# Kernel optimization log

Hardware: AMD Instinct MI355X
Metric: run time of the kernel (lower is better)

The kernel has to match this reference:

```python
import jax, jax.numpy as jnp
import numpy as np

DIM = 256
NUM_HEADS = 8
HEAD_DIM = DIM // NUM_HEADS          # 32
KEY_DIM = int(HEAD_DIM * 0.5)        # 16
SCALE = KEY_DIM ** (-0.5)
QKV_OUT = DIM + 2 * KEY_DIM * NUM_HEADS  # 512
BN_EPS = 1e-3


def _bn(x, gamma, beta, mean, var):
    # inference-mode BatchNorm2d over channel axis 1 of NCHW
    inv = gamma / jnp.sqrt(var + BN_EPS)
    return x * inv[None, :, None, None] + (beta - mean * inv)[None, :, None, None]


def _conv1x1(x, w):
    # w: (O, C, 1, 1)
    return jnp.einsum('bchw,oc->bohw', x, w[:, :, 0, 0])


def _dwconv3x3(x, w):
    # depthwise 3x3, SAME padding; w: (C, 1, 3, 3)
    return jax.lax.conv_general_dilated(
        x, w, window_strides=(1, 1), padding='SAME',
        feature_group_count=x.shape[1],
        dimension_numbers=('NCHW', 'OIHW', 'NCHW'))


def setup_inputs() -> dict:
    key = jax.random.key(0)
    ks = jax.random.split(key, 16)
    B, C, H, W = 16, DIM, 32, 32
    inp = {
        'x': jax.random.normal(ks[0], (B, C, H, W), jnp.float32),
        'qkv_w': jax.random.normal(ks[1], (QKV_OUT, DIM, 1, 1), jnp.float32) * (1.0 / np.sqrt(DIM)),
        'qkv_gamma': jnp.ones((QKV_OUT,), jnp.float32),
        'qkv_beta': jnp.zeros((QKV_OUT,), jnp.float32),
        'qkv_mean': jax.random.normal(ks[2], (QKV_OUT,), jnp.float32) * 0.1,
        'qkv_var': jax.random.uniform(ks[3], (QKV_OUT,), jnp.float32, 0.5, 1.5),
        'pe_w': jax.random.normal(ks[4], (DIM, 1, 3, 3), jnp.float32) * (1.0 / 3.0),
        'pe_gamma': jnp.ones((DIM,), jnp.float32),
        'pe_beta': jnp.zeros((DIM,), jnp.float32),
        'pe_mean': jax.random.normal(ks[5], (DIM,), jnp.float32) * 0.1,
        'pe_var': jax.random.uniform(ks[6], (DIM,), jnp.float32, 0.5, 1.5),
        'proj_w': jax.random.normal(ks[7], (DIM, DIM, 1, 1), jnp.float32) * (1.0 / np.sqrt(DIM)),
        'proj_gamma': jnp.ones((DIM,), jnp.float32),
        'proj_beta': jnp.zeros((DIM,), jnp.float32),
        'proj_mean': jax.random.normal(ks[8], (DIM,), jnp.float32) * 0.1,
        'proj_var': jax.random.uniform(ks[9], (DIM,), jnp.float32, 0.5, 1.5),
    }
    return inp


def reference(x, qkv_w, qkv_gamma, qkv_beta, qkv_mean, qkv_var,
              pe_w, pe_gamma, pe_beta, pe_mean, pe_var,
              proj_w, proj_gamma, proj_beta, proj_mean, proj_var):
    B, C, H, W = x.shape
    N = H * W
    # qkv: 1x1 conv + BN (act=False)
    qkv = _bn(_conv1x1(x, qkv_w), qkv_gamma, qkv_beta, qkv_mean, qkv_var)
    qkv = qkv.reshape(B, NUM_HEADS, 2 * KEY_DIM + HEAD_DIM, N)
    q = qkv[:, :, :KEY_DIM]                          # (B, h, kd, N)
    k = qkv[:, :, KEY_DIM:2 * KEY_DIM]               # (B, h, kd, N)
    v = qkv[:, :, 2 * KEY_DIM:]                      # (B, h, hd, N)
    # attn = (q^T @ k) * scale, softmax over last dim
    attn = jnp.einsum('bhdn,bhdm->bhnm', q, k) * SCALE   # (B, h, N, N)
    attn = jax.nn.softmax(attn, axis=-1)
    # v @ attn^T
    v_attn = jnp.einsum('bhdn,bhmn->bhdm', v, attn)      # (B, h, hd, N)
    v_attn = v_attn.reshape(B, C, H, W)
    v_reshaped = v.reshape(B, C, H, W)
    pos_enc = _bn(_dwconv3x3(v_reshaped, pe_w), pe_gamma, pe_beta, pe_mean, pe_var)
    out = v_attn + pos_enc
    out = _bn(_conv1x1(out, proj_w), proj_gamma, proj_beta, proj_mean, proj_var)
    return out
```

## Files before the change

kernel.cpp:

```cpp
#include <hip/hip_runtime.h>

#define B_ 16
#define C_ 256
#define N_ 1024
#define NH 8
#define HD 32
#define KD 16
#define QKV_OUT_ 512
#define BN_EPS 1e-3f
#define SCALE2_ (0.25f * 1.44269504088896f)

typedef __attribute__((ext_vector_type(8))) short short8;
typedef __attribute__((ext_vector_type(16))) float float16;

__device__ inline unsigned short f2bf(float f) {
  unsigned int u = __float_as_uint(f);
  return (unsigned short)((u + 0x7FFF + ((u >> 16) & 1)) >> 16);
}
__device__ inline float bf2f(unsigned short s) {
  return __uint_as_float(((unsigned int)s) << 16);
}
__device__ inline float16 zero16() {
  float16 z;
  #pragma unroll
  for (int i = 0; i < 16; ++i) z[i] = 0.f;
  return z;
}
__device__ inline unsigned int pack_bf16_trunc(float a, float b) {
  return __builtin_amdgcn_perm(__float_as_uint(b), __float_as_uint(a), 0x07060302u);
}
__device__ inline unsigned int pack_bf16_rne(float a, float b) {
  return (unsigned int)f2bf(a) | ((unsigned int)f2bf(b) << 16);
}
__device__ inline float fast_exp2(float x) {
#if __has_builtin(__builtin_amdgcn_exp2f)
  return __builtin_amdgcn_exp2f(x);
#else
  return exp2f(x);
#endif
}
__device__ inline void pl32(unsigned int& a, unsigned int& b) {
#if __has_builtin(__builtin_amdgcn_permlane32_swap)
  typedef __attribute__((ext_vector_type(2))) int int2v;
  int2v r = __builtin_amdgcn_permlane32_swap((int)a, (int)b, false, false);
  a = (unsigned int)r[0];
  b = (unsigned int)r[1];
#else
  unsigned int ea = (unsigned int)__shfl_xor((int)a, 32, 64);
  unsigned int eb = (unsigned int)__shfl_xor((int)b, 32, 64);
  bool hi = (threadIdx.x & 32) != 0;
  unsigned int an = hi ? eb : a;
  unsigned int bn = hi ? b : ea;
  a = an; b = bn;
#endif
}
__device__ inline short8 lds_frag(const unsigned short* p) {
  union { uint2 u[2]; short8 s; } r;
  r.u[0] = *(const uint2*)p;
  r.u[1] = *(const uint2*)(p + 4);
  return r.s;
}
__device__ inline void lds_store16(unsigned short* p, uint4 v) {
  *(uint2*)p = make_uint2(v.x, v.y);
  *(uint2*)(p + 4) = make_uint2(v.z, v.w);
}
__device__ inline void gl2lds16(const unsigned short* g, unsigned short* l) {
#if __has_builtin(__builtin_amdgcn_global_load_lds)
  __builtin_amdgcn_global_load_lds(
      (const __attribute__((address_space(1))) unsigned int*)g,
      (__attribute__((address_space(3))) unsigned int*)l, 16, 0, 0);
#else
  const int lane = threadIdx.x & 63;
  *(uint4*)((char*)l + lane * 16) = *(const uint4*)g;
#endif
}

__global__ __launch_bounds__(256) void fold_weights(
    const float* __restrict__ qkv_w, const float* __restrict__ qg,
    const float* __restrict__ qb, const float* __restrict__ qm,
    const float* __restrict__ qv,
    const float* __restrict__ proj_w, const float* __restrict__ pg,
    const float* __restrict__ pb, const float* __restrict__ pm,
    const float* __restrict__ pv,
    unsigned short* __restrict__ wq, float* __restrict__ biasq,
    unsigned short* __restrict__ wp, float* __restrict__ biasp)
{
  const int o = blockIdx.x, c = threadIdx.x;
  if (o < QKV_OUT_) {
    float s = ((o & 63) < 16) ? SCALE2_ : 1.f;
    float inv = qg[o] * rsqrtf(qv[o] + BN_EPS) * s;
    wq[o * C_ + c] = f2bf(qkv_w[o * C_ + c] * inv);
    if (c == 0) biasq[o] = qb[o] * s - qm[o] * inv;
  } else {
    int oo = o - QKV_OUT_;
    float inv = pg[oo] * rsqrtf(pv[oo] + BN_EPS);
    wp[oo * C_ + c] = f2bf(proj_w[oo * C_ + c] * inv);
    if (c == 0) biasp[oo] = pb[oo] - pm[oo] * inv;
  }
}

__global__ __launch_bounds__(256) void transpose_x(
    const float* __restrict__ x, unsigned short* __restrict__ xT)
{
  __shared__ float t[64][69];
  const int tid = threadIdx.x;
  const int nt = blockIdx.x, ct = blockIdx.y, b = blockIdx.z;
  const int n0 = nt * 64, c0 = ct * 64;

  #pragma unroll
  for (int it = 0; it < 4; ++it) {
    int cl = it * 16 + (tid >> 4);
    int nl = (tid & 15) * 4;
    float4 v = *(const float4*)(x + ((size_t)b * C_ + c0 + cl) * N_ + n0 + nl);
    t[cl][nl + 0] = v.x; t[cl][nl + 1] = v.y;
    t[cl][nl + 2] = v.z; t[cl][nl + 3] = v.w;
  }
  __syncthreads();

  const int nr = tid >> 2, cseg = (tid & 3) * 16;
  unsigned int pk[8];
  #pragma unroll
  for (int q = 0; q < 8; ++q)
    pk[q] = pack_bf16_rne(t[cseg + 2 * q][nr], t[cseg + 2 * q + 1][nr]);
  unsigned short* row = xT + ((size_t)b * N_ + n0 + nr) * C_ + c0 + cseg;
  *(uint4*)(row)     = make_uint4(pk[0], pk[1], pk[2], pk[3]);
  *(uint4*)(row + 8) = make_uint4(pk[4], pk[5], pk[6], pk[7]);
}

template <int MODE>
__global__ __launch_bounds__(256) void gemm_gl(
    const unsigned short* __restrict__ inT, const unsigned short* __restrict__ wfold,
    const float* __restrict__ bias,
    unsigned short* __restrict__ qkT, unsigned short* __restrict__ vbuf,
    float* __restrict__ outf)
{
  __shared__ __align__(16) unsigned short wa[128 * 64];
  __shared__ __align__(16) unsigned short xb[128 * 64];
  const int tid = threadIdx.x;
  const int wave = tid >> 6, lane = tid & 63, l31 = lane & 31, lh = lane >> 5;
  const int wm = wave & 1, wn = wave >> 1;
  const int n0g = blockIdx.x * 128;
  const int o0 = blockIdx.y * 128;
  const int b = n0g >> 10, nloc = n0g & 1023;

  const int crow = lane >> 3;
  const int cseg = (lane & 7) * 8;

  float16 acc[2][2];
  #pragma unroll
  for (int i = 0; i < 2; ++i)
    #pragma unroll
    for (int j = 0; j < 2; ++j) acc[i][j] = zero16();

  for (int kc = 0; kc < 4; ++kc) {
    __syncthreads();
    #pragma unroll
    for (int j = 0; j < 4; ++j) {
      const int rbase = wave * 32 + j * 8;
      const int row = rbase + crow;
      gl2lds16(wfold + (size_t)(o0 + row) * C_ + kc * 64 + cseg, &wa[rbase * 64]);
      gl2lds16(inT + (size_t)(n0g + row) * C_ + kc * 64 + cseg, &xb[rbase * 64]);
    }
    __syncthreads();

    #pragma unroll
    for (int ks = 0; ks < 4; ++ks) {
      const int ko = ks * 16 + lh * 8;
      short8 a0 = *(const short8*)&wa[(wm * 64 + l31) * 64 + ko];
      short8 a1 = *(const short8*)&wa[(wm * 64 + 32 + l31) * 64 + ko];
      short8 b0 = *(const short8*)&xb[(wn * 64 + l31) * 64 + ko];
      short8 b1 = *(const short8*)&xb[(wn * 64 + 32 + l31) * 64 + ko];
      acc[0][0] = __builtin_amdgcn_mfma_f32_32x32x16_bf16(a0, b0, acc[0][0], 0, 0, 0);
      acc[0][1] = __builtin_amdgcn_mfma_f32_32x32x16_bf16(a0, b1, acc[0][1], 0, 0, 0);
      acc[1][0] = __builtin_amdgcn_mfma_f32_32x32x16_bf16(a1, b0, acc[1][0], 0, 0, 0);
      acc[1][1] = __builtin_amdgcn_mfma_f32_32x32x16_bf16(a1, b1, acc[1][1], 0, 0, 0);
    }
  }

  if constexpr (MODE == 0) {
    const int hh = (o0 >> 6) + wm;
    #pragma unroll
    for (int bn = 0; bn < 2; ++bn) {
      int n = nloc + wn * 64 + bn * 32 + l31;
      unsigned short* row = qkT + (((size_t)b * NH + hh) * N_ + n) * 32;
      #pragma unroll
      for (int qd = 0; qd < 4; ++qd) {
        int cc0 = 8 * qd + 4 * lh;
        ushort4 rv;
        rv.x = f2bf(acc[0][bn][4 * qd + 0] + bias[hh * 64 + cc0 + 0]);
        rv.y = f2bf(acc[0][bn][4 * qd + 1] + bias[hh * 64 + cc0 + 1]);
        rv.z = f2bf(acc[0][bn][4 * qd + 2] + bias[hh * 64 + cc0 + 2]);
        rv.w = f2bf(acc[0][bn][4 * qd + 3] + bias[hh * 64 + cc0 + 3]);
        *(ushort4*)(row + cc0) = rv;
      }
    }
    #pragma unroll
    for (int r = 0; r < 16; ++r) {
      int d = (r & 3) + 8 * (r >> 2) + 4 * lh;
      float bo = bias[hh * 64 + 32 + d];
      unsigned short* vrow =
          vbuf + ((size_t)b * C_ + hh * 32 + d) * N_ + nloc + wn * 64 + l31;
      #pragma unroll
      for (int bn = 0; bn < 2; ++bn)
        vrow[bn * 32] = f2bf(acc[1][bn][r] + bo);
    }
  } else {
    #pragma unroll
    for (int am = 0; am < 2; ++am) {
      #pragma unroll
      for (int r = 0; r < 16; ++r) {
        int o = o0 + wm * 64 + am * 32 + (r & 3) + 8 * (r >> 2) + 4 * lh;
        float bo = bias[o];
        float* orow = outf + ((size_t)b * C_ + o) * N_ + nloc + wn * 64 + l31;
        #pragma unroll
        for (int bn = 0; bn < 2; ++bn)
          orow[bn * 32] = acc[am][bn][r] + bo;
      }
    }
  }
}

__global__ __launch_bounds__(256) void dwconv_bn(
    const unsigned short* __restrict__ vbuf, const float* __restrict__ pw,
    const float* __restrict__ gamma, const float* __restrict__ beta,
    const float* __restrict__ mean, const float* __restrict__ var,
    unsigned short* __restrict__ posb)
{
  __shared__ float t[34][34];
  const int c = blockIdx.x, b = blockIdx.y;
  const int tid = threadIdx.x;
  const unsigned short* vp = vbuf + ((size_t)b * C_ + c) * N_;

  #pragma unroll
  for (int r = 0; r < 4; ++r) {
    int idx = r * 256 + tid;
    t[(idx >> 5) + 1][(idx & 31) + 1] = bf2f(vp[idx]);
  }
  if (tid < 34) {
    t[0][tid] = 0.f; t[33][tid] = 0.f;
    t[tid][0] = 0.f; t[tid][33] = 0.f;
  }
  __syncthreads();

  float w9[9];
  #pragma unroll
  for (int i = 0; i < 9; ++i) w9[i] = pw[c * 9 + i];
  float inv = gamma[c] * rsqrtf(var[c] + BN_EPS);
  float add = beta[c] - mean[c] * inv;

  unsigned short* op = posb + ((size_t)b * C_ + c) * N_;
  #pragma unroll
  for (int r = 0; r < 4; ++r) {
    int idx = r * 256 + tid;
    int y = idx >> 5, x = idx & 31;
    float s = 0.f;
    #pragma unroll
    for (int dy = 0; dy < 3; ++dy)
      #pragma unroll
      for (int dx = 0; dx < 3; ++dx)
        s += t[y + dy][x + dx] * w9[dy * 3 + dx];
    op[idx] = f2bf(s * inv + add);
  }
}

__global__ __launch_bounds__(256) void attn_mfma(
    const unsigned short* __restrict__ qkT, const unsigned short* __restrict__ vbuf,
    const unsigned short* __restrict__ posb, unsigned short* __restrict__ vattnT)
{
  __shared__ __align__(8) unsigned short k_lds[2][128 * 28];
  __shared__ __align__(8) unsigned short v_lds[2][32 * 140];

  const int tid = threadIdx.x;
  const int wave = tid >> 6, lane = tid & 63;
  const int l31 = lane & 31, lh = lane >> 5;
  const int b = blockIdx.x >> 3, h = blockIdx.x & 7;
  const int qbase = blockIdx.y * 128 + wave * 32;

  const unsigned short* qkb = qkT + ((size_t)b * NH + h) * N_ * 32;
  const unsigned short* vhead = vbuf + ((size_t)b * C_ + h * HD) * N_;

  const int skey = tid >> 1, shalf = tid & 1;
  const int svd = tid >> 3, svseg = tid & 7;

  short8 qf = lds_frag(qkb + (size_t)(qbase + l31) * 32 + lh * 8);

  uint4 gk, gv0, gv1;
  auto loadc = [&](int kc) {
    gk  = *(const uint4*)(qkb + (size_t)(kc + skey) * 32 + 16 + shalf * 8);
    gv0 = *(const uint4*)(vhead + (size_t)svd * N_ + kc + svseg * 16);
    gv1 = *(const uint4*)(vhead + (size_t)svd * N_ + kc + svseg * 16 + 8);
  };
  auto storec = [&](int bufi) {
    lds_store16(&k_lds[bufi][skey * 28 + shalf * 8], gk);
    lds_store16(&v_lds[bufi][svd * 140 + svseg * 16], gv0);
    lds_store16(&v_lds[bufi][svd * 140 + svseg * 16 + 8], gv1);
  };

  loadc(0);
  storec(0);
  __syncthreads();

  float16 oacc = zero16();
  float ls[4] = {0.f, 0.f, 0.f, 0.f};

  for (int c = 0; c < 8; ++c) {
    const int buf = c & 1;
    if (c < 7) loadc((c + 1) * 128);

    #pragma unroll
    for (int t = 0; t < 4; ++t) {
      const int key0 = t * 32;
      short8 kf = lds_frag(&k_lds[buf][(key0 + l31) * 28 + lh * 8]);
      float16 st = __builtin_amdgcn_mfma_f32_32x32x16_bf16(kf, qf, zero16(), 0, 0, 0);

      unsigned int u[8];
      #pragma unroll
      for (int q = 0; q < 8; ++q) {
        float pe = fast_exp2(st[2 * q]);
        float po = fast_exp2(st[2 * q + 1]);
        ls[q & 3] += pe + po;
        u[q] = pack_bf16_trunc(pe, po);
      }

      #pragma unroll
      for (int f = 0; f < 2; ++f) {
        short8 vf = lds_frag(&v_lds[buf][l31 * 140 + key0 + f * 16 + lh * 8]);
        const int q0 = f * 4;
        unsigned int a0 = u[q0], a2 = u[q0 + 2]; pl32(a0, a2);
        unsigned int a1 = u[q0 + 1], a3 = u[q0 + 3]; pl32(a1, a3);
        union { unsigned int w[4]; short8 s; } bf;
        bf.w[0] = a0; bf.w[1] = a1; bf.w[2] = a2; bf.w[3] = a3;
        oacc = __builtin_amdgcn_mfma_f32_32x32x16_bf16(vf, bf.s, oacc, 0, 0, 0);
      }
    }

    if (c < 7) storec(buf ^ 1);
    __syncthreads();
  }

  float lsum = (ls[0] + ls[1]) + (ls[2] + ls[3]);
  lsum += __shfl_xor(lsum, 32, 64);
  const float linv = 1.f / lsum;

  const int token = qbase + l31;
  float val[16];
  #pragma unroll
  for (int r = 0; r < 16; ++r) {
    int d = (r & 3) + 8 * (r >> 2) + 4 * lh;
    val[r] = oacc[r] * linv +
             bf2f(posb[((size_t)b * C_ + h * HD + d) * N_ + token]);
  }
  unsigned int u[8];
  #pragma unroll
  for (int m = 0; m < 8; ++m) u[m] = pack_bf16_rne(val[2 * m], val[2 * m + 1]);
  pl32(u[0], u[4]); pl32(u[1], u[5]); pl32(u[2], u[6]); pl32(u[3], u[7]);
  unsigned short* row = vattnT + ((size_t)b * N_ + token) * C_ + h * HD + lh * 16;
  *(uint4*)(row)     = make_uint4(u[0], u[1], u[4], u[5]);
  *(uint4*)(row + 8) = make_uint4(u[2], u[3], u[6], u[7]);
}

extern "C" void kernel_launch(void* const* d_in, const int* in_sizes, int n_in,
                              void* d_out, int out_size, void* d_ws, size_t ws_size,
                              hipStream_t stream) {
  const float* x          = (const float*)d_in[0];
  const float* qkv_w      = (const float*)d_in[1];
  const float* qkv_gamma  = (const float*)d_in[2];
  const float* qkv_beta   = (const float*)d_in[3];
  const float* qkv_mean   = (const float*)d_in[4];
  const float* qkv_var    = (const float*)d_in[5];
  const float* pe_w       = (const float*)d_in[6];
  const float* pe_gamma   = (const float*)d_in[7];
  const float* pe_beta    = (const float*)d_in[8];
  const float* pe_mean    = (const float*)d_in[9];
  const float* pe_var     = (const float*)d_in[10];
  const float* proj_w     = (const float*)d_in[11];
  const float* proj_gamma = (const float*)d_in[12];
  const float* proj_beta  = (const float*)d_in[13];
  const float* proj_mean  = (const float*)d_in[14];
  const float* proj_var   = (const float*)d_in[15];
  float* out = (float*)d_out;

  char* ws = (char*)d_ws;
  unsigned short* qkT = (unsigned short*)ws;
  ws += (size_t)B_ * NH * N_ * 32 * sizeof(unsigned short);
  unsigned short* vbuf = (unsigned short*)ws;
  ws += (size_t)B_ * C_ * N_ * sizeof(unsigned short);
  unsigned short* xT = (unsigned short*)ws;
  ws += (size_t)B_ * N_ * C_ * sizeof(unsigned short);
  unsigned short* vattnT = (unsigned short*)ws;
  ws += (size_t)B_ * N_ * C_ * sizeof(unsigned short);
  unsigned short* posb = (unsigned short*)ws;
  ws += (size_t)B_ * C_ * N_ * sizeof(unsigned short);
  unsigned short* wq = (unsigned short*)ws;
  ws += (size_t)QKV_OUT_ * C_ * sizeof(unsigned short);
  unsigned short* wp = (unsigned short*)ws;
  ws += (size_t)C_ * C_ * sizeof(unsigned short);
  float* biasq = (float*)ws; ws += QKV_OUT_ * sizeof(float);
  float* biasp = (float*)ws;

  fold_weights<<<dim3(QKV_OUT_ + C_), 256, 0, stream>>>(
      qkv_w, qkv_gamma, qkv_beta, qkv_mean, qkv_var,
      proj_w, proj_gamma, proj_beta, proj_mean, proj_var,
      wq, biasq, wp, biasp);

  transpose_x<<<dim3(16, 4, 16), 256, 0, stream>>>(x, xT);

  gemm_gl<0><<<dim3(128, 4), 256, 0, stream>>>(
      xT, wq, biasq, qkT, vbuf, nullptr);

  dwconv_bn<<<dim3(C_, B_), 256, 0, stream>>>(
      vbuf, pe_w, pe_gamma, pe_beta, pe_mean, pe_var, posb);

  attn_mfma<<<dim3(128, 8), 256, 0, stream>>>(qkT, vbuf, posb, vattnT);

  gemm_gl<1><<<dim3(128, 2), 256, 0, stream>>>(
      vattnT, wp, biasp, nullptr, nullptr, out);
}
```

Baseline: 161.1 us.

## Fuse x transpose into QKV GEMM, halve GEMM output tiles, split attn accumulators

```diff
diff --git a/kernel.cpp b/kernel.cpp
--- a/kernel.cpp
+++ b/kernel.cpp
@@ -99,86 +99,59 @@
   }
 }
 
-__global__ __launch_bounds__(256) void transpose_x(
-    const float* __restrict__ x, unsigned short* __restrict__ xT)
+__global__ __launch_bounds__(256) void gemm_qkv(
+    const float* __restrict__ x, const unsigned short* __restrict__ wq,
+    const float* __restrict__ bias,
+    unsigned short* __restrict__ qkT, unsigned short* __restrict__ vbuf)
 {
-  __shared__ float t[64][69];
-  const int tid = threadIdx.x;
-  const int nt = blockIdx.x, ct = blockIdx.y, b = blockIdx.z;
-  const int n0 = nt * 64, c0 = ct * 64;
-
-  #pragma unroll
-  for (int it = 0; it < 4; ++it) {
-    int cl = it * 16 + (tid >> 4);
-    int nl = (tid & 15) * 4;
-    float4 v = *(const float4*)(x + ((size_t)b * C_ + c0 + cl) * N_ + n0 + nl);
-    t[cl][nl + 0] = v.x; t[cl][nl + 1] = v.y;
-    t[cl][nl + 2] = v.z; t[cl][nl + 3] = v.w;
-  }
-  __syncthreads();
-
-  const int nr = tid >> 2, cseg = (tid & 3) * 16;
-  unsigned int pk[8];
-  #pragma unroll
-  for (int q = 0; q < 8; ++q)
-    pk[q] = pack_bf16_rne(t[cseg + 2 * q][nr], t[cseg + 2 * q + 1][nr]);
-  unsigned short* row = xT + ((size_t)b * N_ + n0 + nr) * C_ + c0 + cseg;
-  *(uint4*)(row)     = make_uint4(pk[0], pk[1], pk[2], pk[3]);
-  *(uint4*)(row + 8) = make_uint4(pk[4], pk[5], pk[6], pk[7]);
-}
-
-template <int MODE>
-__global__ __launch_bounds__(256) void gemm_gl(
-    const unsigned short* __restrict__ inT, const unsigned short* __restrict__ wfold,
-    const float* __restrict__ bias,
-    unsigned short* __restrict__ qkT, unsigned short* __restrict__ vbuf,
-    float* __restrict__ outf)
-{
-  __shared__ __align__(16) unsigned short wa[128 * 64];
+  __shared__ __align__(16) unsigned short wa[64 * 64];
   __shared__ __align__(16) unsigned short xb[128 * 64];
   const int tid = threadIdx.x;
   const int wave = tid >> 6, lane = tid & 63, l31 = lane & 31, lh = lane >> 5;
   const int wm = wave & 1, wn = wave >> 1;
-  const int n0g = blockIdx.x * 128;
-  const int o0 = blockIdx.y * 128;
-  const int b = n0g >> 10, nloc = n0g & 1023;
-
-  const int crow = lane >> 3;
-  const int cseg = (lane & 7) * 8;
-
-  float16 acc[2][2];
-  #pragma unroll
-  for (int i = 0; i < 2; ++i)
-    #pragma unroll
-    for (int j = 0; j < 2; ++j) acc[i][j] = zero16();
+  const int b = blockIdx.x >> 3, nloc = (blockIdx.x & 7) * 128;
+  const int hh = blockIdx.y;
+  const int o0 = hh * 64;
+
+  const int tok = tid & 127, ch0 = (tid >> 7) * 32;
+  const float* xcol = x + (size_t)b * C_ * N_ + nloc + tok;
+
+  float16 acc[2];
+  acc[0] = zero16(); acc[1] = zero16();
 
   for (int kc = 0; kc < 4; ++kc) {
     __syncthreads();
     #pragma unroll
-    for (int j = 0; j < 4; ++j) {
-      const int rbase = wave * 32 + j * 8;
-      const int row = rbase + crow;
-      gl2lds16(wfold + (size_t)(o0 + row) * C_ + kc * 64 + cseg, &wa[rbase * 64]);
-      gl2lds16(inT + (size_t)(n0g + row) * C_ + kc * 64 + cseg, &xb[rbase * 64]);
-    }
+    for (int j = 0; j < 2; ++j) {
+      const int rbase = wave * 16 + j * 8;
+      gl2lds16(wq + (size_t)(o0 + rbase + (lane >> 3)) * C_ + kc * 64 + (lane & 7) * 8,
+               &wa[rbase * 64]);
+    }
+    float xv[32];
+    #pragma unroll
+    for (int j = 0; j < 32; ++j)
+      xv[j] = xcol[(size_t)(kc * 64 + ch0 + j) * N_];
+    unsigned int pk[16];
+    #pragma unroll
+    for (int q = 0; q < 16; ++q) pk[q] = pack_bf16_rne(xv[2 * q], xv[2 * q + 1]);
+    #pragma unroll
+    for (int s = 0; s < 4; ++s)
+      *(uint4*)&xb[tok * 64 + ch0 + s * 8] =
+          make_uint4(pk[4 * s], pk[4 * s + 1], pk[4 * s + 2], pk[4 * s + 3]);
     __syncthreads();
 
     #pragma unroll
     for (int ks = 0; ks < 4; ++ks) {
       const int ko = ks * 16 + lh * 8;
-      short8 a0 = *(const short8*)&wa[(wm * 64 + l31) * 64 + ko];
-      short8 a1 = *(const short8*)&wa[(wm * 64 + 32 + l31) * 64 + ko];
+      short8 a0 = *(const short8*)&wa[(wm * 32 + l31) * 64 + ko];
       short8 b0 = *(const short8*)&xb[(wn * 64 + l31) * 64 + ko];
       short8 b1 = *(const short8*)&xb[(wn * 64 + 32 + l31) * 64 + ko];
-      acc[0][0] = __builtin_amdgcn_mfma_f32_32x32x16_bf16(a0, b0, acc[0][0], 0, 0, 0);
-      acc[0][1] = __builtin_amdgcn_mfma_f32_32x32x16_bf16(a0, b1, acc[0][1], 0, 0, 0);
-      acc[1][0] = __builtin_amdgcn_mfma_f32_32x32x16_bf16(a1, b0, acc[1][0], 0, 0, 0);
-      acc[1][1] = __builtin_amdgcn_mfma_f32_32x32x16_bf16(a1, b1, acc[1][1], 0, 0, 0);
-    }
-  }
-
-  if constexpr (MODE == 0) {
-    const int hh = (o0 >> 6) + wm;
+      acc[0] = __builtin_amdgcn_mfma_f32_32x32x16_bf16(a0, b0, acc[0], 0, 0, 0);
+      acc[1] = __builtin_amdgcn_mfma_f32_32x32x16_bf16(a0, b1, acc[1], 0, 0, 0);
+    }
+  }
+
+  if (wm == 0) {
     #pragma unroll
     for (int bn = 0; bn < 2; ++bn) {
       int n = nloc + wn * 64 + bn * 32 + l31;
@@ -187,13 +160,14 @@
       for (int qd = 0; qd < 4; ++qd) {
         int cc0 = 8 * qd + 4 * lh;
         ushort4 rv;
-        rv.x = f2bf(acc[0][bn][4 * qd + 0] + bias[hh * 64 + cc0 + 0]);
-        rv.y = f2bf(acc[0][bn][4 * qd + 1] + bias[hh * 64 + cc0 + 1]);
-        rv.z = f2bf(acc[0][bn][4 * qd + 2] + bias[hh * 64 + cc0 + 2]);
-        rv.w = f2bf(acc[0][bn][4 * qd + 3] + bias[hh * 64 + cc0 + 3]);
+        rv.x = f2bf(acc[bn][4 * qd + 0] + bias[hh * 64 + cc0 + 0]);
+        rv.y = f2bf(acc[bn][4 * qd + 1] + bias[hh * 64 + cc0 + 1]);
+        rv.z = f2bf(acc[bn][4 * qd + 2] + bias[hh * 64 + cc0 + 2]);
+        rv.w = f2bf(acc[bn][4 * qd + 3] + bias[hh * 64 + cc0 + 3]);
         *(ushort4*)(row + cc0) = rv;
       }
     }
+  } else {
     #pragma unroll
     for (int r = 0; r < 16; ++r) {
       int d = (r & 3) + 8 * (r >> 2) + 4 * lh;
@@ -202,21 +176,62 @@
           vbuf + ((size_t)b * C_ + hh * 32 + d) * N_ + nloc + wn * 64 + l31;
       #pragma unroll
       for (int bn = 0; bn < 2; ++bn)
-        vrow[bn * 32] = f2bf(acc[1][bn][r] + bo);
-    }
-  } else {
-    #pragma unroll
-    for (int am = 0; am < 2; ++am) {
-      #pragma unroll
-      for (int r = 0; r < 16; ++r) {
-        int o = o0 + wm * 64 + am * 32 + (r & 3) + 8 * (r >> 2) + 4 * lh;
-        float bo = bias[o];
-        float* orow = outf + ((size_t)b * C_ + o) * N_ + nloc + wn * 64 + l31;
-        #pragma unroll
-        for (int bn = 0; bn < 2; ++bn)
-          orow[bn * 32] = acc[am][bn][r] + bo;
-      }
-    }
+        vrow[bn * 32] = f2bf(acc[bn][r] + bo);
+    }
+  }
+}
+
+__global__ __launch_bounds__(256) void gemm_proj(
+    const unsigned short* __restrict__ inT, const unsigned short* __restrict__ wp,
+    const float* __restrict__ bias, float* __restrict__ outf)
+{
+  __shared__ __align__(16) unsigned short wa[64 * 64];
+  __shared__ __align__(16) unsigned short xb[128 * 64];
+  const int tid = threadIdx.x;
+  const int wave = tid >> 6, lane = tid & 63, l31 = lane & 31, lh = lane >> 5;
+  const int wm = wave & 1, wn = wave >> 1;
+  const int n0g = blockIdx.x * 128;
+  const int o0 = blockIdx.y * 64;
+  const int b = n0g >> 10, nloc = n0g & 1023;
+
+  float16 acc[2];
+  acc[0] = zero16(); acc[1] = zero16();
+
+  for (int kc = 0; kc < 4; ++kc) {
+    __syncthreads();
+    #pragma unroll
+    for (int j = 0; j < 2; ++j) {
+      const int rbase = wave * 16 + j * 8;
+      gl2lds16(wp + (size_t)(o0 + rbase + (lane >> 3)) * C_ + kc * 64 + (lane & 7) * 8,
+               &wa[rbase * 64]);
+    }
+    #pragma unroll
+    for (int j = 0; j < 4; ++j) {
+      const int rbase = wave * 32 + j * 8;
+      gl2lds16(inT + (size_t)(n0g + rbase + (lane >> 3)) * C_ + kc * 64 + (lane & 7) * 8,
+               &xb[rbase * 64]);
+    }
+    __syncthreads();
+
+    #pragma unroll
+    for (int ks = 0; ks < 4; ++ks) {
+      const int ko = ks * 16 + lh * 8;
+      short8 a0 = *(const short8*)&wa[(wm * 32 + l31) * 64 + ko];
+      short8 b0 = *(const short8*)&xb[(wn * 64 + l31) * 64 + ko];
+      short8 b1 = *(const short8*)&xb[(wn * 64 + 32 + l31) * 64 + ko];
+      acc[0] = __builtin_amdgcn_mfma_f32_32x32x16_bf16(a0, b0, acc[0], 0, 0, 0);
+      acc[1] = __builtin_amdgcn_mfma_f32_32x32x16_bf16(a0, b1, acc[1], 0, 0, 0);
+    }
+  }
+
+  #pragma unroll
+  for (int r = 0; r < 16; ++r) {
+    int o = o0 + wm * 32 + (r & 3) + 8 * (r >> 2) + 4 * lh;
+    float bo = bias[o];
+    float* orow = outf + ((size_t)b * C_ + o) * N_ + nloc + wn * 64 + l31;
+    #pragma unroll
+    for (int bn = 0; bn < 2; ++bn)
+      orow[bn * 32] = acc[bn][r] + bo;
   }
 }
 
@@ -300,7 +315,7 @@
   storec(0);
   __syncthreads();
 
-  float16 oacc = zero16();
+  float16 oaccE = zero16(), oaccO = zero16();
   float ls[4] = {0.f, 0.f, 0.f, 0.f};
 
   for (int c = 0; c < 8; ++c) {
@@ -330,7 +345,10 @@
         unsigned int a1 = u[q0 + 1], a3 = u[q0 + 3]; pl32(a1, a3);
         union { unsigned int w[4]; short8 s; } bf;
         bf.w[0] = a0; bf.w[1] = a1; bf.w[2] = a2; bf.w[3] = a3;
-        oacc = __builtin_amdgcn_mfma_f32_32x32x16_bf16(vf, bf.s, oacc, 0, 0, 0);
+        if (f == 0)
+          oaccE = __builtin_amdgcn_mfma_f32_32x32x16_bf16(vf, bf.s, oaccE, 0, 0, 0);
+        else
+          oaccO = __builtin_amdgcn_mfma_f32_32x32x16_bf16(vf, bf.s, oaccO, 0, 0, 0);
       }
     }
 
@@ -347,7 +365,7 @@
   #pragma unroll
   for (int r = 0; r < 16; ++r) {
     int d = (r & 3) + 8 * (r >> 2) + 4 * lh;
-    val[r] = oacc[r] * linv +
+    val[r] = (oaccE[r] + oaccO[r]) * linv +
              bf2f(posb[((size_t)b * C_ + h * HD + d) * N_ + token]);
   }
   unsigned int u[8];
@@ -385,8 +403,6 @@
   ws += (size_t)B_ * NH * N_ * 32 * sizeof(unsigned short);
   unsigned short* vbuf = (unsigned short*)ws;
   ws += (size_t)B_ * C_ * N_ * sizeof(unsigned short);
-  unsigned short* xT = (unsigned short*)ws;
-  ws += (size_t)B_ * N_ * C_ * sizeof(unsigned short);
   unsigned short* vattnT = (unsigned short*)ws;
   ws += (size_t)B_ * N_ * C_ * sizeof(unsigned short);
   unsigned short* posb = (unsigned short*)ws;
@@ -403,16 +419,12 @@
       proj_w, proj_gamma, proj_beta, proj_mean, proj_var,
       wq, biasq, wp, biasp);
 
-  transpose_x<<<dim3(16, 4, 16), 256, 0, stream>>>(x, xT);
-
-  gemm_gl<0><<<dim3(128, 4), 256, 0, stream>>>(
-      xT, wq, biasq, qkT, vbuf, nullptr);
+  gemm_qkv<<<dim3(128, 8), 256, 0, stream>>>(x, wq, biasq, qkT, vbuf);
 
   dwconv_bn<<<dim3(C_, B_), 256, 0, stream>>>(
       vbuf, pe_w, pe_gamma, pe_beta, pe_mean, pe_var, posb);
 
   attn_mfma<<<dim3(128, 8), 256, 0, stream>>>(qkT, vbuf, posb, vattnT);
 
-  gemm_gl<1><<<dim3(128, 2), 256, 0, stream>>>(
-      vattnT, wp, biasp, nullptr, nullptr, out);
-}
+  gemm_proj<<<dim3(128, 4), 256, 0, stream>>>(vattnT, wp, biasp, out);
+}
```

Result: slower. 166.1 us (+3.2%).
